# Kernel tuning notes

Hardware: AMD Instinct MI355X
Metric: run time of the kernel (lower is better)

## Reference

```python
import jax, jax.numpy as jnp
import numpy as np

B, T, C, NH, L, V = 2, 1024, 768, 12, 4, 50304
HS = C // NH  # 64


def _norm(x):
    # torch: (x - x.mean(-1)) / x.std(-1) with unbiased std (ddof=1)
    mu = jnp.mean(x, axis=-1, keepdims=True)
    sd = jnp.std(x, axis=-1, ddof=1, keepdims=True)
    return (x - mu) / sd


def setup_inputs() -> dict:
    key = jax.random.key(0)
    ks = jax.random.split(key, 8)
    idx = jax.random.randint(ks[0], (B, T), 0, V)
    wte = jax.random.normal(ks[1], (V, C), jnp.float32) * 0.02
    wpe = jax.random.normal(ks[2], (1024, C), jnp.float32) * 0.02
    c_attn_w = jax.random.normal(ks[3], (L, 3 * C, C), jnp.float32) * 0.02
    c_proj_w = jax.random.normal(ks[4], (L, C, C), jnp.float32) * 0.02
    w_decay = jax.random.uniform(ks[5], (L, C), jnp.float32)          # decay in [0,1)
    eta = jax.random.uniform(ks[6], (L, C), jnp.float32) * 0.01       # small, like 1/block_size init
    lm_head_w = jax.random.normal(ks[7], (V, C), jnp.float32) * 0.02
    return dict(idx=idx, wte=wte, wpe=wpe, c_attn_w=c_attn_w, c_proj_w=c_proj_w,
                w_decay=w_decay, eta=eta, lm_head_w=lm_head_w)


def _rwkv7_block(x, Wqkv, Wproj, wd, et):
    Bx, Tx, Cx = x.shape
    qkv = (x @ Wqkv.T).reshape(Bx, Tx, 3, NH, HS)
    qkv = _norm(qkv)
    # [T, B, nh, hs] each
    q = jnp.transpose(qkv[:, :, 0], (1, 0, 2, 3))
    k = jnp.transpose(qkv[:, :, 1], (1, 0, 2, 3))
    v = jnp.transpose(qkv[:, :, 2], (1, 0, 2, 3))
    q = jax.lax.erf(q)
    k = jax.lax.erf(k)
    wv = wd.reshape(NH, HS)   # decay per (head, channel i)
    ev = et.reshape(NH, HS)
    a = -k
    b = k * ev
    k_ = k * ev
    v_ = v

    def step(state, inp):
        q_t, a_t, b_t, k_t, v_t = inp
        # state: [B, nh, hs(i), hs(k)]
        sab = jnp.einsum('bhik,bhk,bhj->bhij', state, a_t, b_t)
        state = state * wv[None, :, :, None] + sab + jnp.einsum('bhj,bhi->bhij', k_t, v_t)
        out = jnp.einsum('bhj,bhij->bhi', q_t, state)
        return state, out

    state0 = jnp.zeros((Bx, NH, HS, HS), x.dtype)
    _, vt = jax.lax.scan(step, state0, (q, a, b, k_, v_))  # vt: [T, B, nh, hs]
    y = jnp.transpose(vt, (1, 0, 2, 3)).reshape(Bx, Tx, Cx) @ Wproj.T
    return x + y


def reference(idx, wte, wpe, c_attn_w, c_proj_w, w_decay, eta, lm_head_w):
    t = idx.shape[1]
    x = wte[idx] + wpe[:t][None]
    for l in range(L):
        x = _rwkv7_block(x, c_attn_w[l], c_proj_w[l], w_decay[l], eta[l])
    x = _norm(x)
    # targets=None path: logits for last position only
    logits = x[:, -1:, :] @ lm_head_w.T  # [B, 1, V]
    return logits
```

## Files before the change

### kernel.cpp

```cpp
#include <hip/hip_runtime.h>
#include <hip/hip_bf16.h>
#include <cmath>

using bf16   = __bf16;
using bf16x8 = __attribute__((ext_vector_type(8))) __bf16;
using bf16x4 = __attribute__((ext_vector_type(4))) __bf16;
using f32x4  = __attribute__((ext_vector_type(4))) float;
using u32x4  = __attribute__((ext_vector_type(4))) unsigned int;

__global__ __launch_bounds__(256) void cast4_kernel(const float* __restrict__ src,
                                                    bf16* __restrict__ dst, int n4) {
  int i = blockIdx.x * 256 + threadIdx.x;
  int stride = gridDim.x * 256;
  for (; i < n4; i += stride) {
    f32x4 v = ((const f32x4*)src)[i];
    bf16x4 o;
    o[0] = (bf16)v[0]; o[1] = (bf16)v[1]; o[2] = (bf16)v[2]; o[3] = (bf16)v[3];
    ((bf16x4*)dst)[i] = o;
  }
}

__global__ __launch_bounds__(256) void emb_kernel(const int* __restrict__ idx,
                                                  const float* __restrict__ wte,
                                                  const float* __restrict__ wpe,
                                                  float* __restrict__ xf,
                                                  bf16* __restrict__ xb) {
  int bt = blockIdx.x;
  int t = bt & 1023;
  int tok = idx[bt];
  const float* wr = wte + (long)tok * 768;
  const float* pr = wpe + (long)t * 768;
  for (int c = threadIdx.x; c < 768; c += 256) {
    float v = wr[c] + pr[c];
    xf[(long)bt * 768 + c] = v;
    xb[(long)bt * 768 + c] = (bf16)v;
  }
}

template <int PROJ>
__global__ __launch_bounds__(256) void gemm_kernel(const bf16* __restrict__ A,
                                                   const bf16* __restrict__ W,
                                                   float* __restrict__ out,
                                                   float* __restrict__ xf,
                                                   bf16* __restrict__ xb,
                                                   int N, int K) {
  __shared__ char ldsA[128 * 128];
  __shared__ char ldsB[128 * 128];
  const int tid = threadIdx.x;
  const int l = tid & 63, wid = tid >> 6;
  const int lr = l & 15, g = l >> 4;
  const int m0 = blockIdx.y * 128, n0 = blockIdx.x * 128;
  const int wm = wid >> 1, wn = wid & 1;

  f32x4 acc[4][4];
#pragma unroll
  for (int i = 0; i < 4; ++i)
#pragma unroll
    for (int j = 0; j < 4; ++j) acc[i][j] = {0.f, 0.f, 0.f, 0.f};

  for (int k0 = 0; k0 < K; k0 += 32) {
    __syncthreads();
#pragma unroll
    for (int it = 0; it < 2; ++it) {
      int slot = tid + it * 256;
      int row = slot >> 2, q = slot & 3;
      u32x4 da = *(const u32x4*)(A + (long)(m0 + row) * K + k0 + q * 8);
      *(u32x4*)(ldsA + row * 128 + ((q * 16) ^ ((row & 7) << 4))) = da;
      u32x4 db = *(const u32x4*)(W + (long)(n0 + row) * K + k0 + q * 8);
      *(u32x4*)(ldsB + row * 128 + ((q * 16) ^ ((row & 7) << 4))) = db;
    }
    __syncthreads();
    bf16x8 af[4], bfr[4];
#pragma unroll
    for (int it = 0; it < 4; ++it) {
      int row = wm * 64 + it * 16 + lr;
      af[it] = *(const bf16x8*)(ldsA + row * 128 + ((16 * g) ^ ((row & 7) << 4)));
    }
#pragma unroll
    for (int jt = 0; jt < 4; ++jt) {
      int row = wn * 64 + jt * 16 + lr;
      bfr[jt] = *(const bf16x8*)(ldsB + row * 128 + ((16 * g) ^ ((row & 7) << 4)));
    }
#pragma unroll
    for (int it = 0; it < 4; ++it)
#pragma unroll
      for (int jt = 0; jt < 4; ++jt)
        acc[it][jt] = __builtin_amdgcn_mfma_f32_16x16x32_bf16(af[it], bfr[jt], acc[it][jt], 0, 0, 0);
  }

#pragma unroll
  for (int it = 0; it < 4; ++it) {
#pragma unroll
    for (int jt = 0; jt < 4; ++jt) {
      int col = n0 + wn * 64 + jt * 16 + lr;
#pragma unroll
      for (int r = 0; r < 4; ++r) {
        int row = m0 + wm * 64 + it * 16 + g * 4 + r;
        if constexpr (PROJ) {
          long o = (long)row * 768 + col;
          float v = acc[it][jt][r] + xf[o];
          xf[o] = v;
          xb[o] = (bf16)v;
        } else {
          out[(long)row * N + col] = acc[it][jt][r];
        }
      }
    }
  }
}

__global__ __launch_bounds__(256) void normgram_kernel(const float* __restrict__ qkv,
                                                       const float* __restrict__ eta_l,
                                                       bf16* __restrict__ qG,
                                                       bf16* __restrict__ aG,
                                                       float* __restrict__ vG,
                                                       float* __restrict__ GaG,
                                                       bf16* __restrict__ GqG,
                                                       bf16* __restrict__ bTG) {
  const int bh = blockIdx.x >> 6, ch = blockIdx.x & 63;
  const int b = bh / 12, h = bh - b * 12;
  const int tid = threadIdx.x;
  __shared__ float raw[48][68];
  __shared__ float as[16][68], bs[16][68], qs[16][68];

  const long qbase = ((long)(b * 1024 + ch * 16)) * 2304 + h * 64;
#pragma unroll
  for (int i = 0; i < 3; ++i) {
    int slot = tid + i * 256;
    int c4 = slot & 15, sgrp = slot >> 4;
    int t = sgrp / 3, s = sgrp - 3 * t;
    f32x4 d = *(const f32x4*)(qkv + qbase + (long)t * 2304 + s * 768 + c4 * 4);
    *(f32x4*)(&raw[sgrp][c4 * 4]) = d;
  }
  __syncthreads();

  const int l = tid & 63, w = tid >> 6;
  const float ev = eta_l[h * 64 + l];
#pragma unroll
  for (int j = 0; j < 12; ++j) {
    int sgrp = w * 12 + j;
    int t = sgrp / 3, s = sgrp - 3 * t;
    float x = raw[sgrp][l];
    float mu = x;
#pragma unroll
    for (int o = 32; o; o >>= 1) mu += __shfl_xor(mu, o);
    mu *= (1.f / 64.f);
    float d = x - mu;
    float v2 = d * d;
#pragma unroll
    for (int o = 32; o; o >>= 1) v2 += __shfl_xor(v2, o);
    float sd = sqrtf(v2 * (1.f / 63.f));
    float gn = d / sd;
    long rowb = ((long)bh * 1024 + ch * 16 + t) * 64;
    if (s == 0) {
      float qv = erff(gn);
      qs[t][l] = qv;
      qG[rowb + l] = (bf16)qv;
    } else if (s == 1) {
      float kh = erff(gn);
      as[t][l] = -kh;
      bs[t][l] = kh * ev;
      aG[rowb + l] = (bf16)(-kh);
    } else {
      vG[rowb + l] = gn;
    }
  }
  __syncthreads();

  const int t = tid & 15, u = tid >> 4;
  float dba = 0.f, dbq = 0.f;
#pragma unroll 4
  for (int d = 0; d < 64; ++d) {
    float bv = bs[u][d];
    dba += bv * as[t][d];
    dbq += bv * qs[t][d];
  }
  long g2 = (long)bh * 64 + ch;
  GaG[g2 * 256 + u * 16 + t] = (u < t) ? dba : 0.f;
  GqG[g2 * 512 + t * 32 + u] = (u <= t) ? (bf16)dbq : (bf16)0.f;
  GqG[g2 * 512 + t * 32 + 16 + u] = (bf16)0.f;
  int jj = tid >> 2, uq = tid & 3;
  bf16x8 pkv;
#pragma unroll
  for (int uu = 0; uu < 8; ++uu) pkv[uu] = (uq < 2) ? (bf16)bs[uq * 8 + uu][jj] : (bf16)0.f;
  *(bf16x8*)(bTG + g2 * 2048 + jj * 32 + uq * 8) = pkv;
}

__global__ __launch_bounds__(64) void scan_kernel(const float* __restrict__ wdl,
                                                  const bf16* __restrict__ aG,
                                                  const bf16* __restrict__ qG,
                                                  const float* __restrict__ vG,
                                                  const float* __restrict__ GaG,
                                                  const bf16* __restrict__ GqG,
                                                  const bf16* __restrict__ bTG,
                                                  bf16* __restrict__ yG) {
  const int bid = blockIdx.x;
  const int bh = bid % 24, qi = bid / 24;
  const int b = bh / 12, h = bh - b * 12;
  const int i0 = qi * 16;
  const int l = threadIdx.x;
  const int g = l >> 4, lr = l & 15;

  __shared__ char  sA[2][16 * 128];
  __shared__ char  sQ[2][16 * 128];
  __shared__ char  sB[2][64 * 64];
  __shared__ char  sG[2][16 * 64];
  __shared__ float sGa[2][16][16];
  __shared__ float sV[2][16][16];
  __shared__ char  sS[16 * 128];
  __shared__ float sM[16][17];

  const float* wrow = wdl + h * 64;
  const float w_rec = fmaxf(wrow[i0 + lr], 0.004f);
  const float winv = 1.0f / w_rec;

  float wc[4], w15c[4], l2wc[4];
#pragma unroll
  for (int r = 0; r < 4; ++r) {
    float w = fmaxf(wrow[i0 + g * 4 + r], 0.004f);
    wc[r] = w;
    l2wc[r] = log2f(w);
    w15c[r] = exp2f(15.0f * l2wc[r]);
  }

  f32x4 Sf[4];
#pragma unroll
  for (int j = 0; j < 4; ++j) Sf[j] = {0.f, 0.f, 0.f, 0.f};

  const long hTD = (long)bh * 65536;
  const long gB = (long)bh * 64;
  const int tr = l >> 2, tq = l & 3;

  u32x4 rA0, rA1, rQ0, rQ1, rB[4], rGq;
  f32x4 rGa, rV;

  auto LOAD = [&](int c) {
    const long tb = hTD + (long)c * 1024;
    const bf16* ap = aG + tb + tr * 64 + tq * 16;
    rA0 = *(const u32x4*)(ap);
    rA1 = *(const u32x4*)(ap + 8);
    const bf16* qp = qG + tb + tr * 64 + tq * 16;
    rQ0 = *(const u32x4*)(qp);
    rQ1 = *(const u32x4*)(qp + 8);
    const bf16* bp = bTG + (gB + c) * 2048 + l * 32;
#pragma unroll
    for (int k = 0; k < 4; ++k) rB[k] = *(const u32x4*)(bp + k * 8);
    rGq = *(const u32x4*)(GqG + (gB + c) * 512 + tr * 32 + tq * 8);
    rGa = *(const f32x4*)(GaG + (gB + c) * 256 + l * 4);
    rV = *(const f32x4*)(vG + tb + tr * 64 + i0 + tq * 4);
  };

  auto STORE = [&](int nb) {
    const int swzr = (tr & 7) << 4;
    *(u32x4*)(sA[nb] + tr * 128 + ((tq * 32) ^ swzr)) = rA0;
    *(u32x4*)(sA[nb] + tr * 128 + ((tq * 32 + 16) ^ swzr)) = rA1;
    *(u32x4*)(sQ[nb] + tr * 128 + ((tq * 32) ^ swzr)) = rQ0;
    *(u32x4*)(sQ[nb] + tr * 128 + ((tq * 32 + 16) ^ swzr)) = rQ1;
#pragma unroll
    for (int k = 0; k < 4; ++k)
      *(u32x4*)(sB[nb] + l * 64 + ((k * 16) ^ ((l & 3) << 4))) = rB[k];
    *(u32x4*)(sG[nb] + tr * 64 + ((tq * 16) ^ ((tr & 3) << 4))) = rGq;
    *(f32x4*)(&sGa[nb][tr][tq * 4]) = rGa;
    *(f32x4*)(&sV[nb][tr][tq * 4]) = rV;
  };

  LOAD(0);
  STORE(0);
#pragma unroll
  for (int jt = 0; jt < 4; ++jt) {
#pragma unroll
    for (int r = 0; r < 4; ++r) {
      int row = g * 4 + r;
      int d = jt * 16 + lr;
      *(bf16*)(sS + row * 128 + ((d * 2) ^ ((row & 7) << 4))) = (bf16)0.0f;
    }
  }

  int cur = 0;
  for (int c = 0; c < 64; ++c) {
    asm volatile("s_waitcnt lgkmcnt(0)" ::: "memory");
    __builtin_amdgcn_sched_barrier(0);

    if (c < 63) LOAD(c + 1);

    const int swz7 = (lr & 7) << 4, swz3 = (lr & 3) << 4;
    f32x4 mf = {0.f, 0.f, 0.f, 0.f}, mqf = {0.f, 0.f, 0.f, 0.f};
#pragma unroll
    for (int s = 0; s < 2; ++s) {
      bf16x8 af = *(const bf16x8*)(sS + lr * 128 + ((64 * s + 16 * g) ^ swz7));
      bf16x8 ba = *(const bf16x8*)(sA[cur] + lr * 128 + ((64 * s + 16 * g) ^ swz7));
      bf16x8 bq = *(const bf16x8*)(sQ[cur] + lr * 128 + ((64 * s + 16 * g) ^ swz7));
      mf = __builtin_amdgcn_mfma_f32_16x16x32_bf16(af, ba, mf, 0, 0, 0);
      mqf = __builtin_amdgcn_mfma_f32_16x16x32_bf16(af, bq, mqf, 0, 0, 0);
    }
#pragma unroll
    for (int r = 0; r < 4; ++r) sM[lr][g * 4 + r] = mf[r];
    asm volatile("s_waitcnt lgkmcnt(0)" ::: "memory");
    __builtin_amdgcn_sched_barrier(0);

    f32x4 acc4[4];
#pragma unroll
    for (int t = 0; t < 4; ++t) acc4[t] = {0.f, 0.f, 0.f, 0.f};
    bf16x8 zfrag;
#pragma unroll
    for (int i = 0; i < 8; ++i) zfrag[i] = (bf16)0.0f;
    float wp = 1.f, wpm1 = 0.f, wiv = 1.f;
#pragma unroll
    for (int u = 0; u < 16; ++u) {
      float muv = sM[u][lr];
      float vu = sV[cur][u][lr];
      float cc = wp * muv + wpm1 * acc4[u >> 2][u & 3];
      float zt = wiv * (cc + vu);
      zfrag[u & 7] = (g == (u >> 3)) ? (bf16)zt : zfrag[u & 7];
      f32x4 ztv = {zt, zt, zt, zt};
#pragma unroll
      for (int qq = 0; qq < 4; ++qq) {
        f32x4 ga = *(const f32x4*)(&sGa[cur][u][qq * 4]);
        acc4[qq] = __builtin_elementwise_fma(ga, ztv, acc4[qq]);
      }
      wpm1 = wp;
      wp *= w_rec;
      wiv *= winv;
    }

    if (c < 63) STORE(cur ^ 1);

#pragma unroll
    for (int jt = 0; jt < 4; ++jt) {
      int jrow = jt * 16 + lr;
      bf16x8 bb = *(const bf16x8*)(sB[cur] + jrow * 64 + ((16 * g) ^ ((jrow & 3) << 4)));
      f32x4 cs;
#pragma unroll
      for (int r = 0; r < 4; ++r) cs[r] = Sf[jt][r] * wc[r];
      f32x4 ns = __builtin_amdgcn_mfma_f32_16x16x32_bf16(zfrag, bb, cs, 0, 0, 0);
#pragma unroll
      for (int r = 0; r < 4; ++r) Sf[jt][r] = ns[r] * w15c[r];
    }

#pragma unroll
    for (int jt = 0; jt < 4; ++jt) {
#pragma unroll
      for (int r = 0; r < 4; ++r) {
        int row = g * 4 + r;
        int d = jt * 16 + lr;
        *(bf16*)(sS + row * 128 + ((d * 2) ^ ((row & 7) << 4))) = (bf16)Sf[jt][r];
      }
    }

    {
      bf16x8 gq = *(const bf16x8*)(sG[cur] + lr * 64 + ((16 * g) ^ swz3));
      f32x4 cy;
#pragma unroll
      for (int r = 0; r < 4; ++r) cy[r] = mqf[r] * wc[r];
      f32x4 yp = __builtin_amdgcn_mfma_f32_16x16x32_bf16(zfrag, gq, cy, 0, 0, 0);
      bf16x4 yo;
#pragma unroll
      for (int r = 0; r < 4; ++r) yo[r] = (bf16)(yp[r] * exp2f((float)lr * l2wc[r]));
      long yoff = ((long)b * 1024 + c * 16 + lr) * 768 + h * 64 + i0 + g * 4;
      *(bf16x4*)(yG + yoff) = yo;
    }

    cur ^= 1;
  }
}

__global__ __launch_bounds__(256) void finalnorm_kernel(const float* __restrict__ xf,
                                                        float* __restrict__ xn) {
  __shared__ float red[4];
  int tid = threadIdx.x;
  for (int b = 0; b < 2; ++b) {
    const float* xr = xf + ((long)b * 1024 + 1023) * 768;
    float s = 0.f;
    for (int c = tid; c < 768; c += 256) s += xr[c];
#pragma unroll
    for (int o = 32; o; o >>= 1) s += __shfl_xor(s, o);
    if ((tid & 63) == 0) red[tid >> 6] = s;
    __syncthreads();
    float mu = (red[0] + red[1] + red[2] + red[3]) * (1.f / 768.f);
    __syncthreads();
    float s2 = 0.f;
    for (int c = tid; c < 768; c += 256) {
      float d = xr[c] - mu;
      s2 += d * d;
    }
#pragma unroll
    for (int o = 32; o; o >>= 1) s2 += __shfl_xor(s2, o);
    if ((tid & 63) == 0) red[tid >> 6] = s2;
    __syncthreads();
    float sd = sqrtf((red[0] + red[1] + red[2] + red[3]) * (1.f / 767.f));
    for (int c = tid; c < 768; c += 256) xn[b * 768 + c] = (xr[c] - mu) / sd;
    __syncthreads();
  }
}

__global__ __launch_bounds__(256) void lmhead_kernel(const float* __restrict__ W,
                                                     const float* __restrict__ xn,
                                                     float* __restrict__ out) {
  int l = threadIdx.x & 63, wid = threadIdx.x >> 6;
  int v0 = blockIdx.x * 64 + wid * 16;
  f32x4 x0[3], x1[3];
#pragma unroll
  for (int i = 0; i < 3; ++i) {
    x0[i] = *(const f32x4*)(xn + l * 4 + i * 256);
    x1[i] = *(const f32x4*)(xn + 768 + l * 4 + i * 256);
  }
  for (int vi = 0; vi < 16; ++vi) {
    const float* wr = W + (long)(v0 + vi) * 768;
    float pa = 0.f, pb = 0.f;
#pragma unroll
    for (int i = 0; i < 3; ++i) {
      f32x4 wv = *(const f32x4*)(wr + l * 4 + i * 256);
#pragma unroll
      for (int r = 0; r < 4; ++r) {
        pa += wv[r] * x0[i][r];
        pb += wv[r] * x1[i][r];
      }
    }
#pragma unroll
    for (int o = 32; o; o >>= 1) {
      pa += __shfl_xor(pa, o);
      pb += __shfl_xor(pb, o);
    }
    if (l == 0) {
      out[v0 + vi] = pa;
      out[50304 + v0 + vi] = pb;
    }
  }
}

extern "C" void kernel_launch(void* const* d_in, const int* in_sizes, int n_in,
                              void* d_out, int out_size, void* d_ws, size_t ws_size,
                              hipStream_t stream) {
  (void)in_sizes; (void)n_in; (void)out_size; (void)ws_size;
  const int*   idx      = (const int*)d_in[0];
  const float* wte      = (const float*)d_in[1];
  const float* wpe      = (const float*)d_in[2];
  const float* c_attn_w = (const float*)d_in[3];
  const float* c_proj_w = (const float*)d_in[4];
  const float* w_decay  = (const float*)d_in[5];
  const float* eta      = (const float*)d_in[6];
  const float* lm_head  = (const float*)d_in[7];
  float* out = (float*)d_out;

  char* ws = (char*)d_ws;
  size_t off = 0;
  auto alloc = [&](size_t bytes) -> char* {
    char* p = ws + off;
    off = (off + bytes + 255) & ~(size_t)255;
    return p;
  };
  float* xf   = (float*)alloc(2L * 1024 * 768 * 4);
  bf16*  xb   = (bf16*)alloc(2L * 1024 * 768 * 2);
  float* qkv  = (float*)alloc(2L * 1024 * 2304 * 4);
  bf16*  qGp  = (bf16*)alloc(24L * 1024 * 64 * 2);
  bf16*  aGp  = (bf16*)alloc(24L * 1024 * 64 * 2);
  float* vGp  = (float*)alloc(24L * 1024 * 64 * 4);
  float* GaGp = (float*)alloc(24L * 64 * 256 * 4);
  bf16*  GqGp = (bf16*)alloc(24L * 64 * 512 * 2);
  bf16*  bTGp = (bf16*)alloc(24L * 64 * 2048 * 2);
  bf16*  yGp  = (bf16*)alloc(2L * 1024 * 768 * 2);
  bf16*  WqB  = (bf16*)alloc(4L * 2304 * 768 * 2);
  bf16*  WpB  = (bf16*)alloc(4L * 768 * 768 * 2);
  float* xn   = (float*)alloc(2L * 768 * 4);

  cast4_kernel<<<dim3(2048), dim3(256), 0, stream>>>(c_attn_w, WqB, 4 * 2304 * 768 / 4);
  cast4_kernel<<<dim3(1024), dim3(256), 0, stream>>>(c_proj_w, WpB, 4 * 768 * 768 / 4);
  emb_kernel<<<dim3(2048), dim3(256), 0, stream>>>(idx, wte, wpe, xf, xb);

  for (int l = 0; l < 4; ++l) {
    gemm_kernel<0><<<dim3(18, 16), dim3(256), 0, stream>>>(
        xb, WqB + (long)l * 2304 * 768, qkv, nullptr, nullptr, 2304, 768);
    normgram_kernel<<<dim3(1536), dim3(256), 0, stream>>>(
        qkv, eta + l * 768, qGp, aGp, vGp, GaGp, GqGp, bTGp);
    scan_kernel<<<dim3(96), dim3(64), 0, stream>>>(
        w_decay + l * 768, aGp, qGp, vGp, GaGp, GqGp, bTGp, yGp);
    gemm_kernel<1><<<dim3(6, 16), dim3(256), 0, stream>>>(
        yGp, WpB + (long)l * 768 * 768, nullptr, xf, xb, 768, 768);
  }

  finalnorm_kernel<<<dim3(1), dim3(256), 0, stream>>>(xf, xn);
  lmhead_kernel<<<dim3(786), dim3(256), 0, stream>>>(lm_head, xn, out);
}
```

Before: 921.0 us.

## Merge four scan row-blocks per head into one workgroup sharing staged chunk data

The scan kernel drops from 96 single-wave blocks to 12 blocks of 512 threads. Each block handles two (batch, head) pairs with four waves per head, and each wave owns 16 state rows. The per-chunk A/Q/B/G/V tiles are now loaded once per head into shared memory and shared by the four waves, instead of each wave reloading the same data, and the full 64-row state lives in shared memory. This adds a __syncthreads per chunk and leaves only 12 workgroups active, so most CUs sit idle, in exchange for less redundant global traffic.

After: 868.0 us. -5.8%, faster.

```diff
diff --git a/kernel.cpp b/kernel.cpp
--- a/kernel.cpp
+++ b/kernel.cpp
@@ -186,38 +186,42 @@
   *(bf16x8*)(bTG + g2 * 2048 + jj * 32 + uq * 8) = pkv;
 }
 
-__global__ __launch_bounds__(64) void scan_kernel(const float* __restrict__ wdl,
-                                                  const bf16* __restrict__ aG,
-                                                  const bf16* __restrict__ qG,
-                                                  const float* __restrict__ vG,
-                                                  const float* __restrict__ GaG,
-                                                  const bf16* __restrict__ GqG,
-                                                  const bf16* __restrict__ bTG,
-                                                  bf16* __restrict__ yG) {
-  const int bid = blockIdx.x;
-  const int bh = bid % 24, qi = bid / 24;
+__global__ __launch_bounds__(512) void scan_kernel(const float* __restrict__ wdl,
+                                                   const bf16* __restrict__ aG,
+                                                   const bf16* __restrict__ qG,
+                                                   const float* __restrict__ vG,
+                                                   const float* __restrict__ GaG,
+                                                   const bf16* __restrict__ GqG,
+                                                   const bf16* __restrict__ bTG,
+                                                   bf16* __restrict__ yG) {
+  const int tid = threadIdx.x;
+  const int hb = tid >> 8;
+  const int tloc = tid & 255;
+  const int w4 = (tid >> 6) & 3;
+  const int l = tid & 63;
+  const int lr = l & 15, g = l >> 4;
+  const int bh = blockIdx.x * 2 + hb;
   const int b = bh / 12, h = bh - b * 12;
-  const int i0 = qi * 16;
-  const int l = threadIdx.x;
-  const int g = l >> 4, lr = l & 15;
-
-  __shared__ char  sA[2][16 * 128];
-  __shared__ char  sQ[2][16 * 128];
-  __shared__ char  sB[2][64 * 64];
-  __shared__ char  sG[2][16 * 64];
-  __shared__ float sGa[2][16][16];
-  __shared__ float sV[2][16][16];
-  __shared__ char  sS[16 * 128];
-  __shared__ float sM[16][17];
+
+  __shared__ char  sA[2][2][16 * 128];
+  __shared__ char  sQ[2][2][16 * 128];
+  __shared__ char  sB[2][2][64 * 64];
+  __shared__ char  sG[2][2][16 * 64];
+  __shared__ float sGa[2][2][16][16];
+  __shared__ float sV[2][2][16][64];
+  __shared__ char  sS[2][64 * 128];
+  __shared__ float sM[2][16][68];
 
   const float* wrow = wdl + h * 64;
-  const float w_rec = fmaxf(wrow[i0 + lr], 0.004f);
+  const int irow = w4 * 16 + lr;
+  const float w_rec = fmaxf(wrow[irow], 0.004f);
   const float winv = 1.0f / w_rec;
 
   float wc[4], w15c[4], l2wc[4];
 #pragma unroll
   for (int r = 0; r < 4; ++r) {
-    float w = fmaxf(wrow[i0 + g * 4 + r], 0.004f);
+    int row = w4 * 16 + g * 4 + r;
+    float w = fmaxf(wrow[row], 0.004f);
     wc[r] = w;
     l2wc[r] = log2f(w);
     w15c[r] = exp2f(15.0f * l2wc[r]);
@@ -229,39 +233,49 @@
 
   const long hTD = (long)bh * 65536;
   const long gB = (long)bh * 64;
-  const int tr = l >> 2, tq = l & 3;
-
-  u32x4 rA0, rA1, rQ0, rQ1, rB[4], rGq;
-  f32x4 rGa, rV;
+
+  u32x4 rAQ, rB, rGG;
+  f32x4 rV;
 
   auto LOAD = [&](int c) {
     const long tb = hTD + (long)c * 1024;
-    const bf16* ap = aG + tb + tr * 64 + tq * 16;
-    rA0 = *(const u32x4*)(ap);
-    rA1 = *(const u32x4*)(ap + 8);
-    const bf16* qp = qG + tb + tr * 64 + tq * 16;
-    rQ0 = *(const u32x4*)(qp);
-    rQ1 = *(const u32x4*)(qp + 8);
-    const bf16* bp = bTG + (gB + c) * 2048 + l * 32;
-#pragma unroll
-    for (int k = 0; k < 4; ++k) rB[k] = *(const u32x4*)(bp + k * 8);
-    rGq = *(const u32x4*)(GqG + (gB + c) * 512 + tr * 32 + tq * 8);
-    rGa = *(const f32x4*)(GaG + (gB + c) * 256 + l * 4);
-    rV = *(const f32x4*)(vG + tb + tr * 64 + i0 + tq * 4);
+    if (tloc < 128) {
+      rAQ = *(const u32x4*)(aG + tb + (tloc >> 3) * 64 + (tloc & 7) * 8);
+    } else {
+      rAQ = *(const u32x4*)(qG + tb + ((tloc - 128) >> 3) * 64 + ((tloc - 128) & 7) * 8);
+    }
+    rB = *(const u32x4*)(bTG + (gB + c) * 2048 + (tloc >> 2) * 32 + (tloc & 3) * 8);
+    if (tloc < 64) {
+      rGG = *(const u32x4*)(GqG + (gB + c) * 512 + (tloc >> 2) * 32 + (tloc & 3) * 8);
+    } else if (tloc < 128) {
+      rGG = *(const u32x4*)(GaG + (gB + c) * 256 + ((tloc - 64) >> 2) * 16 + ((tloc - 64) & 3) * 4);
+    }
+    rV = *(const f32x4*)(vG + tb + (tloc >> 4) * 64 + (tloc & 15) * 4);
   };
 
   auto STORE = [&](int nb) {
-    const int swzr = (tr & 7) << 4;
-    *(u32x4*)(sA[nb] + tr * 128 + ((tq * 32) ^ swzr)) = rA0;
-    *(u32x4*)(sA[nb] + tr * 128 + ((tq * 32 + 16) ^ swzr)) = rA1;
-    *(u32x4*)(sQ[nb] + tr * 128 + ((tq * 32) ^ swzr)) = rQ0;
-    *(u32x4*)(sQ[nb] + tr * 128 + ((tq * 32 + 16) ^ swzr)) = rQ1;
-#pragma unroll
-    for (int k = 0; k < 4; ++k)
-      *(u32x4*)(sB[nb] + l * 64 + ((k * 16) ^ ((l & 3) << 4))) = rB[k];
-    *(u32x4*)(sG[nb] + tr * 64 + ((tq * 16) ^ ((tr & 3) << 4))) = rGq;
-    *(f32x4*)(&sGa[nb][tr][tq * 4]) = rGa;
-    *(f32x4*)(&sV[nb][tr][tq * 4]) = rV;
+    if (tloc < 128) {
+      int t = tloc >> 3, q = tloc & 7;
+      *(u32x4*)(sA[hb][nb] + t * 128 + ((q * 16) ^ ((t & 7) << 4))) = rAQ;
+    } else {
+      int t = (tloc - 128) >> 3, q = (tloc - 128) & 7;
+      *(u32x4*)(sQ[hb][nb] + t * 128 + ((q * 16) ^ ((t & 7) << 4))) = rAQ;
+    }
+    {
+      int j = tloc >> 2, q = tloc & 3;
+      *(u32x4*)(sB[hb][nb] + j * 64 + ((q * 16) ^ ((j & 3) << 4))) = rB;
+    }
+    if (tloc < 64) {
+      int t = tloc >> 2, q = tloc & 3;
+      *(u32x4*)(sG[hb][nb] + t * 64 + ((q * 16) ^ ((t & 3) << 4))) = rGG;
+    } else if (tloc < 128) {
+      int u = (tloc - 64) >> 2, q = (tloc - 64) & 3;
+      *(u32x4*)(&sGa[hb][nb][u][q * 4]) = rGG;
+    }
+    {
+      int t = tloc >> 4, i4 = tloc & 15;
+      *(f32x4*)(&sV[hb][nb][t][i4 * 4]) = rV;
+    }
   };
 
   LOAD(0);
@@ -270,31 +284,31 @@
   for (int jt = 0; jt < 4; ++jt) {
 #pragma unroll
     for (int r = 0; r < 4; ++r) {
-      int row = g * 4 + r;
+      int row = w4 * 16 + g * 4 + r;
       int d = jt * 16 + lr;
-      *(bf16*)(sS + row * 128 + ((d * 2) ^ ((row & 7) << 4))) = (bf16)0.0f;
-    }
-  }
-
-  int cur = 0;
+      *(bf16*)(sS[hb] + row * 128 + ((d * 2) ^ ((row & 7) << 4))) = (bf16)0.0f;
+    }
+  }
+  __syncthreads();
+
   for (int c = 0; c < 64; ++c) {
+    const int cur = c & 1;
+    if (c < 63) LOAD(c + 1);
+
     asm volatile("s_waitcnt lgkmcnt(0)" ::: "memory");
     __builtin_amdgcn_sched_barrier(0);
 
-    if (c < 63) LOAD(c + 1);
-
-    const int swz7 = (lr & 7) << 4, swz3 = (lr & 3) << 4;
     f32x4 mf = {0.f, 0.f, 0.f, 0.f}, mqf = {0.f, 0.f, 0.f, 0.f};
 #pragma unroll
     for (int s = 0; s < 2; ++s) {
-      bf16x8 af = *(const bf16x8*)(sS + lr * 128 + ((64 * s + 16 * g) ^ swz7));
-      bf16x8 ba = *(const bf16x8*)(sA[cur] + lr * 128 + ((64 * s + 16 * g) ^ swz7));
-      bf16x8 bq = *(const bf16x8*)(sQ[cur] + lr * 128 + ((64 * s + 16 * g) ^ swz7));
+      bf16x8 af = *(const bf16x8*)(sS[hb] + irow * 128 + ((64 * s + 16 * g) ^ ((irow & 7) << 4)));
+      bf16x8 ba = *(const bf16x8*)(sA[hb][cur] + lr * 128 + ((64 * s + 16 * g) ^ ((lr & 7) << 4)));
+      bf16x8 bq = *(const bf16x8*)(sQ[hb][cur] + lr * 128 + ((64 * s + 16 * g) ^ ((lr & 7) << 4)));
       mf = __builtin_amdgcn_mfma_f32_16x16x32_bf16(af, ba, mf, 0, 0, 0);
       mqf = __builtin_amdgcn_mfma_f32_16x16x32_bf16(af, bq, mqf, 0, 0, 0);
     }
 #pragma unroll
-    for (int r = 0; r < 4; ++r) sM[lr][g * 4 + r] = mf[r];
+    for (int r = 0; r < 4; ++r) sM[hb][lr][w4 * 16 + g * 4 + r] = mf[r];
     asm volatile("s_waitcnt lgkmcnt(0)" ::: "memory");
     __builtin_amdgcn_sched_barrier(0);
 
@@ -307,15 +321,15 @@
     float wp = 1.f, wpm1 = 0.f, wiv = 1.f;
 #pragma unroll
     for (int u = 0; u < 16; ++u) {
-      float muv = sM[u][lr];
-      float vu = sV[cur][u][lr];
+      float muv = sM[hb][u][irow];
+      float vu = sV[hb][cur][u][irow];
       float cc = wp * muv + wpm1 * acc4[u >> 2][u & 3];
       float zt = wiv * (cc + vu);
       zfrag[u & 7] = (g == (u >> 3)) ? (bf16)zt : zfrag[u & 7];
       f32x4 ztv = {zt, zt, zt, zt};
 #pragma unroll
       for (int qq = 0; qq < 4; ++qq) {
-        f32x4 ga = *(const f32x4*)(&sGa[cur][u][qq * 4]);
+        f32x4 ga = *(const f32x4*)(&sGa[hb][cur][u][qq * 4]);
         acc4[qq] = __builtin_elementwise_fma(ga, ztv, acc4[qq]);
       }
       wpm1 = wp;
@@ -323,12 +337,10 @@
       wiv *= winv;
     }
 
-    if (c < 63) STORE(cur ^ 1);
-
 #pragma unroll
     for (int jt = 0; jt < 4; ++jt) {
       int jrow = jt * 16 + lr;
-      bf16x8 bb = *(const bf16x8*)(sB[cur] + jrow * 64 + ((16 * g) ^ ((jrow & 3) << 4)));
+      bf16x8 bb = *(const bf16x8*)(sB[hb][cur] + jrow * 64 + ((16 * g) ^ ((jrow & 3) << 4)));
       f32x4 cs;
 #pragma unroll
       for (int r = 0; r < 4; ++r) cs[r] = Sf[jt][r] * wc[r];
@@ -341,14 +353,14 @@
     for (int jt = 0; jt < 4; ++jt) {
 #pragma unroll
       for (int r = 0; r < 4; ++r) {
-        int row = g * 4 + r;
+        int row = w4 * 16 + g * 4 + r;
         int d = jt * 16 + lr;
-        *(bf16*)(sS + row * 128 + ((d * 2) ^ ((row & 7) << 4))) = (bf16)Sf[jt][r];
+        *(bf16*)(sS[hb] + row * 128 + ((d * 2) ^ ((row & 7) << 4))) = (bf16)Sf[jt][r];
       }
     }
 
     {
-      bf16x8 gq = *(const bf16x8*)(sG[cur] + lr * 64 + ((16 * g) ^ swz3));
+      bf16x8 gq = *(const bf16x8*)(sG[hb][cur] + lr * 64 + ((16 * g) ^ ((lr & 3) << 4)));
       f32x4 cy;
 #pragma unroll
       for (int r = 0; r < 4; ++r) cy[r] = mqf[r] * wc[r];
@@ -356,11 +368,12 @@
       bf16x4 yo;
 #pragma unroll
       for (int r = 0; r < 4; ++r) yo[r] = (bf16)(yp[r] * exp2f((float)lr * l2wc[r]));
-      long yoff = ((long)b * 1024 + c * 16 + lr) * 768 + h * 64 + i0 + g * 4;
+      long yoff = ((long)b * 1024 + c * 16 + lr) * 768 + h * 64 + w4 * 16 + g * 4;
       *(bf16x4*)(yG + yoff) = yo;
     }
 
-    cur ^= 1;
+    if (c < 63) STORE(cur ^ 1);
+    __syncthreads();
   }
 }
 
@@ -472,7 +485,7 @@
         xb, WqB + (long)l * 2304 * 768, qkv, nullptr, nullptr, 2304, 768);
     normgram_kernel<<<dim3(1536), dim3(256), 0, stream>>>(
         qkv, eta + l * 768, qGp, aGp, vGp, GaGp, GqGp, bTGp);
-    scan_kernel<<<dim3(96), dim3(64), 0, stream>>>(
+    scan_kernel<<<dim3(12), dim3(512), 0, stream>>>(
         w_decay + l * 768, aGp, qGp, vGp, GaGp, GqGp, bTGp, yGp);
     gemm_kernel<1><<<dim3(6, 16), dim3(256), 0, stream>>>(
         yGp, WpB + (long)l * 768 * 768, nullptr, xf, xb, 768, 768);
```
